# Kernel optimization log

Measured on AMD Instinct MI355X. Metric: run time of the kernel, lower is better.

Reference implementation:

```python
import jax, jax.numpy as jnp
import numpy as np

H = 1024      # hidden_size
I = 512       # moe_intermediate_size
E = 8         # n_routed_experts
K = 2         # num_experts_per_tok
SI = I * 2    # shared expert intermediate (n_shared_experts=2)
B, S = 2, 1024


def setup_inputs() -> dict:
    key = jax.random.key(0)
    ks = jax.random.split(key, 9)
    s = 0.02
    return {
        "x": jax.random.normal(ks[0], (B, S, H), jnp.float32),
        "gate_w": jax.random.normal(ks[1], (E, H), jnp.float32) * s,
        "lb_bias": jnp.zeros((E,), jnp.float32),
        "expert_gate_w": jax.random.normal(ks[2], (E, I, H), jnp.float32) * s,
        "expert_up_w": jax.random.normal(ks[3], (E, I, H), jnp.float32) * s,
        "expert_down_w": jax.random.normal(ks[4], (E, H, I), jnp.float32) * s,
        "shared_gate_w": jax.random.normal(ks[5], (SI, H), jnp.float32) * s,
        "shared_up_w": jax.random.normal(ks[6], (SI, H), jnp.float32) * s,
        "shared_down_w": jax.random.normal(ks[7], (H, SI), jnp.float32) * s,
    }


def _mlp(x, gw, uw, dw):
    # SwiGLU: down( silu(gate(x)) * up(x) )
    return (jax.nn.silu(x @ gw.T) * (x @ uw.T)) @ dw.T


def reference(x, gate_w, lb_bias, expert_gate_w, expert_up_w, expert_down_w,
              shared_gate_w, shared_up_w, shared_down_w):
    b, s, h = x.shape
    xf = x.reshape(-1, h)                                   # [T, H]
    # --- SimpleRouter (sigmoid scoring) ---
    logits = xf @ gate_w.T + lb_bias                        # [T, E]
    scores = jax.nn.sigmoid(logits.astype(jnp.float32))
    topw, topi = jax.lax.top_k(scores, K)                   # [T, K]
    topw = (topw / (topw.sum(-1, keepdims=True) + 1e-8)).astype(x.dtype)
    # --- _process_local: per-expert dispatch/compute/combine ---
    # Faithful to torch source: expert_weights[mask].mean(dim=-1) collapses to a
    # SCALAR per expert (mean routing weight over all tokens sent to that expert).
    out = jnp.zeros_like(xf)
    for e in range(E):
        m = (topi == e)                                     # [T, K]
        sel = m.any(axis=-1)                                # [T]
        cnt = m.sum()
        wmean = (topw * m).sum() / jnp.maximum(cnt, 1).astype(topw.dtype)
        y = _mlp(xf, expert_gate_w[e], expert_up_w[e], expert_down_w[e])  # [T, H]
        out = out + jnp.where(sel[:, None], y * wmean, jnp.zeros((), x.dtype))
    out = out.reshape(b, s, h)
    # --- shared experts ---
    out = out + _mlp(x, shared_gate_w, shared_up_w, shared_down_w)
    return out
```

## Files before the change

### kernel.cpp

```cpp
#include <hip/hip_runtime.h>

#define H_DIM 1024
#define I_DIM 512
#define NE 8
#define SI_DIM 1024
#define NT 2048
#define NS 4096

typedef __bf16 bf16;
typedef __bf16 bf16x4 __attribute__((ext_vector_type(4)));
typedef __bf16 bf16x8 __attribute__((ext_vector_type(8)));
typedef float f32x4 __attribute__((ext_vector_type(4)));

#define OFF_CNT 0
#define OFF_WM 64
#define OFF_TOPI 1024
#define OFF_TOPW (OFF_TOPI + NT * 8)
#define OFF_LISTS (OFF_TOPW + NT * 8)
#define OFF_XB (OFF_LISTS + NE * NT * 4)
#define OFF_ACTE (OFF_XB + (size_t)NT * H_DIM * 2)
#define OFF_ACTS (OFF_ACTE + (size_t)NE * NT * I_DIM * 2)

__device__ __forceinline__ bf16x4 cvt4(f32x4 v) {
  bf16x4 r;
  r.x = (bf16)v.x; r.y = (bf16)v.y; r.z = (bf16)v.z; r.w = (bf16)v.w;
  return r;
}

__device__ __forceinline__ bf16x8 cvt8(f32x4 a, f32x4 b) {
  bf16x8 r;
  r[0] = (bf16)a.x; r[1] = (bf16)a.y; r[2] = (bf16)a.z; r[3] = (bf16)a.w;
  r[4] = (bf16)b.x; r[5] = (bf16)b.y; r[6] = (bf16)b.z; r[7] = (bf16)b.w;
  return r;
}

__device__ __forceinline__ void glds16(const bf16* g, bf16* l) {
  __builtin_amdgcn_global_load_lds(
      (const __attribute__((address_space(1))) unsigned int*)g,
      (__attribute__((address_space(3))) unsigned int*)l, 16, 0, 0);
}

__global__ __launch_bounds__(256) void router_kernel(
    const float* __restrict__ x, const float* __restrict__ gw,
    const float* __restrict__ lb, bf16* __restrict__ xb,
    int2* __restrict__ topi, float2* __restrict__ topw) {
  const int lane = threadIdx.x & 63;
  const int t = blockIdx.x * 4 + (threadIdx.x >> 6);
  const float* xr = x + (size_t)t * H_DIM;
  bf16* xw = xb + (size_t)t * H_DIM;

  float s[NE];
#pragma unroll
  for (int e = 0; e < NE; e++) s[e] = 0.f;
#pragma unroll
  for (int k0 = 0; k0 < H_DIM; k0 += 256) {
    f32x4 xv = *(const f32x4*)(xr + k0 + lane * 4);
    *(bf16x4*)(xw + k0 + lane * 4) = cvt4(xv);
#pragma unroll
    for (int e = 0; e < NE; e++) {
      f32x4 gv = *(const f32x4*)(gw + e * H_DIM + k0 + lane * 4);
      s[e] += xv.x * gv.x + xv.y * gv.y + xv.z * gv.z + xv.w * gv.w;
    }
  }
#pragma unroll
  for (int e = 0; e < NE; e++) {
    float v = s[e];
#pragma unroll
    for (int off = 32; off > 0; off >>= 1) v += __shfl_xor(v, off);
    s[e] = v;
  }
  if (lane == 0) {
    float sc[NE];
#pragma unroll
    for (int e = 0; e < NE; e++) sc[e] = 1.f / (1.f + expf(-(s[e] + lb[e])));
    int i1 = 0;
#pragma unroll
    for (int e = 1; e < NE; e++)
      if (sc[e] > sc[i1]) i1 = e;
    int i2 = -1;
#pragma unroll
    for (int e = 0; e < NE; e++) {
      if (e == i1) continue;
      if (i2 < 0 || sc[e] > sc[i2]) i2 = e;
    }
    float w1 = sc[i1], w2 = sc[i2];
    float inv = 1.f / (w1 + w2 + 1e-8f);
    topi[t] = make_int2(i1, i2);
    topw[t] = make_float2(w1 * inv, w2 * inv);
  }
}

__global__ __launch_bounds__(256) void build_kernel(
    const int2* __restrict__ topi, const float2* __restrict__ topw,
    int* __restrict__ cnt, float* __restrict__ wm, int* __restrict__ lists) {
  const int e = blockIdx.x;
  const int wave = threadIdx.x >> 6, lane = threadIdx.x & 63;
  __shared__ int wc[4];
  __shared__ float wf[4];
  const int tbeg = wave * (NT / 4), tend = tbeg + NT / 4;

  int c = 0;
  float wa = 0.f;
  for (int t0 = tbeg; t0 < tend; t0 += 64) {
    int2 ti = topi[t0 + lane];
    float2 tw = topw[t0 + lane];
    bool hit = (ti.x == e) || (ti.y == e);
    float w = (ti.x == e) ? tw.x : ((ti.y == e) ? tw.y : 0.f);
    c += __popcll(__ballot(hit));
#pragma unroll
    for (int off = 32; off > 0; off >>= 1) w += __shfl_xor(w, off);
    wa += w;
  }
  if (lane == 0) { wc[wave] = c; wf[wave] = wa; }
  __syncthreads();
  int pos = 0;
  for (int w = 0; w < wave; w++) pos += wc[w];
  for (int t0 = tbeg; t0 < tend; t0 += 64) {
    int t = t0 + lane;
    int2 ti = topi[t];
    bool hit = (ti.x == e) || (ti.y == e);
    unsigned long long m = __ballot(hit);
    int pre = __popcll(m & ((1ull << lane) - 1ull));
    if (hit) lists[e * NT + pos + pre] = t;
    pos += __popcll(m);
  }
  if (threadIdx.x == 0) {
    int ctot = wc[0] + wc[1] + wc[2] + wc[3];
    cnt[e] = ctot;
    wm[e] = (wf[0] + wf[1] + wf[2] + wf[3]) / (float)(ctot > 0 ? ctot : 1);
  }
}

__global__ __launch_bounds__(256, 2) void gemm_gu(
    const float* __restrict__ eg, const float* __restrict__ eu,
    const float* __restrict__ sg, const float* __restrict__ su,
    const bf16* __restrict__ xb, const int* __restrict__ cnt,
    const int* __restrict__ lists, bf16* __restrict__ act_e,
    bf16* __restrict__ act_s) {
  const int z = blockIdx.z, ct = blockIdx.x, rt = blockIdx.y;
  const int tid = threadIdx.x;
  __shared__ int rows_s[128];
  __shared__ __align__(16) bf16 As[128 * 64];
  __shared__ __align__(16) bf16 Bs[128 * 64];
  int mrem, ldc;
  bf16* Cb;
  const float *Pg, *Pu;
  if (z < NE) {
    if (ct >= 8) return;
    int c = cnt[z];
    if (rt * 128 >= c) return;
    mrem = c - rt * 128;
    if (tid < 128)
      rows_s[tid] = lists[z * NT + rt * 128 + (tid < mrem ? tid : mrem - 1)];
    Pg = eg + ((size_t)z << 19);
    Pu = eu + ((size_t)z << 19);
    Cb = act_e + ((size_t)z * NT + rt * 128) * I_DIM;
    ldc = I_DIM;
  } else {
    mrem = 128;
    if (tid < 128) rows_s[tid] = rt * 128 + tid;
    Pg = sg;
    Pu = su;
    Cb = act_s + (size_t)rt * 128 * SI_DIM;
    ldc = SI_DIM;
  }
  __syncthreads();

  const int lane = tid & 63, wave = tid >> 6;
  const int mw = (wave >> 1) * 64, nw = (wave & 1) * 64;
  const int l15 = lane & 15, quad = lane >> 4;
  const int srow = tid >> 3;
  const int cch = tid & 7;
  const int p8 = cch * 8;
  const int sx = (l15 & 7) * 8;
  const int ctb = ct * 128;

  const bf16* ap[4];
  const float* bp[4];
  int alo[4], blo[4];
#pragma unroll
  for (int r = 0; r < 4; r++) {
    int R = srow + r * 32;
    ap[r] = xb + (size_t)rows_s[R] * H_DIM + ((cch ^ (R & 7)) * 8);
    alo[r] = R * 64 + p8;
    int idx = ctb + R;
    int b = idx >> 4;
    int sr = ((b >> 1) << 4) | (idx & 15);
    bp[r] = ((b & 1) ? Pu : Pg) + (size_t)sr * H_DIM + p8;
    blo[r] = R * 64 + ((cch ^ (R & 7)) * 8);
  }

  f32x4 acc[4][4] = {};
  for (int k0 = 0; k0 < H_DIM; k0 += 64) {
#pragma unroll
    for (int r = 0; r < 4; r++) glds16(ap[r] + k0, &As[alo[r]]);
#pragma unroll
    for (int r = 0; r < 4; r++) {
      f32x4 v0 = *(const f32x4*)(bp[r] + k0);
      f32x4 v1 = *(const f32x4*)(bp[r] + k0 + 4);
      *(bf16x8*)&Bs[blo[r]] = cvt8(v0, v1);
    }
    __syncthreads();
#pragma unroll
    for (int kk = 0; kk < 2; kk++) {
      const int ko = (kk * 4 + quad) * 8;
      bf16x8 av[4], bv[4];
#pragma unroll
      for (int i = 0; i < 4; i++) {
        av[i] = *(const bf16x8*)&As[(mw + i * 16 + l15) * 64 + (ko ^ sx)];
        bv[i] = *(const bf16x8*)&Bs[(nw + i * 16 + l15) * 64 + (ko ^ sx)];
      }
#pragma unroll
      for (int i = 0; i < 4; i++)
#pragma unroll
        for (int j = 0; j < 4; j++)
          acc[i][j] = __builtin_amdgcn_mfma_f32_16x16x32_bf16(av[i], bv[j], acc[i][j], 0, 0, 0);
    }
    __syncthreads();
  }

#pragma unroll
  for (int i = 0; i < 4; i++) {
#pragma unroll
    for (int rg = 0; rg < 4; rg++) {
      int rl = mw + i * 16 + quad * 4 + rg;
      if (rl < mrem) {
#pragma unroll
        for (int jp = 0; jp < 2; jp++) {
          float g = acc[i][jp * 2][rg];
          float u = acc[i][jp * 2 + 1][rg];
          int c = ct * 64 + (nw >> 1) + jp * 16 + l15;
          Cb[(size_t)rl * ldc + c] = (bf16)((g / (1.f + __expf(-g))) * u);
        }
      }
    }
  }
}

__global__ __launch_bounds__(256, 2) void gemm_down(
    const float* __restrict__ ed, const float* __restrict__ sd,
    const bf16* __restrict__ act_e, const bf16* __restrict__ act_s,
    const int* __restrict__ cnt, const float* __restrict__ wm,
    const int* __restrict__ lists, float* __restrict__ out) {
  const int z = blockIdx.z, ct = blockIdx.x, rt = blockIdx.y;
  const int tid = threadIdx.x;
  __shared__ int rows_s[128];
  __shared__ __align__(16) bf16 As[128 * 64];
  __shared__ __align__(16) bf16 Bs[128 * 64];
  int K, mrem;
  const bf16* Ab;
  const float* Bbase;
  if (z < NE) {
    int c = cnt[z];
    if (rt * 128 >= c) return;
    mrem = c - rt * 128;
    if (tid < 128)
      rows_s[tid] = lists[z * NT + rt * 128 + (tid < mrem ? tid : mrem - 1)];
    Ab = act_e + ((size_t)z * NT + rt * 128) * I_DIM;
    K = I_DIM;
    Bbase = ed + (size_t)z * H_DIM * I_DIM;
  } else {
    mrem = 128;
    if (tid < 128) rows_s[tid] = rt * 128 + tid;
    Ab = act_s + (size_t)rt * 128 * SI_DIM;
    K = SI_DIM;
    Bbase = sd;
  }
  __syncthreads();

  const int lane = tid & 63, wave = tid >> 6;
  const int mw = (wave >> 1) * 64, nw = (wave & 1) * 64;
  const int l15 = lane & 15, quad = lane >> 4;
  const int srow = tid >> 3;
  const int cch = tid & 7;
  const int p8 = cch * 8;
  const int sx = (l15 & 7) * 8;

  const bf16* ap[4];
  const float* bp[4];
  int alo[4], blo[4];
#pragma unroll
  for (int r = 0; r < 4; r++) {
    int R = srow + r * 32;
    ap[r] = Ab + (size_t)R * K + ((cch ^ (R & 7)) * 8);
    alo[r] = R * 64 + p8;
    bp[r] = Bbase + (size_t)(ct * 128 + R) * K + p8;
    blo[r] = R * 64 + ((cch ^ (R & 7)) * 8);
  }

  f32x4 acc[4][4] = {};
  for (int k0 = 0; k0 < K; k0 += 64) {
#pragma unroll
    for (int r = 0; r < 4; r++) glds16(ap[r] + k0, &As[alo[r]]);
#pragma unroll
    for (int r = 0; r < 4; r++) {
      f32x4 v0 = *(const f32x4*)(bp[r] + k0);
      f32x4 v1 = *(const f32x4*)(bp[r] + k0 + 4);
      *(bf16x8*)&Bs[blo[r]] = cvt8(v0, v1);
    }
    __syncthreads();
#pragma unroll
    for (int kk = 0; kk < 2; kk++) {
      const int ko = (kk * 4 + quad) * 8;
      bf16x8 av[4], bv[4];
#pragma unroll
      for (int i = 0; i < 4; i++) {
        av[i] = *(const bf16x8*)&As[(mw + i * 16 + l15) * 64 + (ko ^ sx)];
        bv[i] = *(const bf16x8*)&Bs[(nw + i * 16 + l15) * 64 + (ko ^ sx)];
      }
#pragma unroll
      for (int i = 0; i < 4; i++)
#pragma unroll
        for (int j = 0; j < 4; j++)
          acc[i][j] = __builtin_amdgcn_mfma_f32_16x16x32_bf16(av[i], bv[j], acc[i][j], 0, 0, 0);
    }
    __syncthreads();
  }

  const float wsc = (z < NE) ? wm[z] : 1.f;
#pragma unroll
  for (int i = 0; i < 4; i++) {
#pragma unroll
    for (int rg = 0; rg < 4; rg++) {
      int rl = mw + i * 16 + quad * 4 + rg;
      if (rl < mrem) {
        int t = rows_s[rl];
        float* orow = out + (size_t)t * H_DIM + ct * 128 + nw;
#pragma unroll
        for (int j = 0; j < 4; j++)
          atomicAdd(&orow[j * 16 + l15], wsc * acc[i][j][rg]);
      }
    }
  }
}

extern "C" void kernel_launch(void* const* d_in, const int* in_sizes, int n_in,
                              void* d_out, int out_size, void* d_ws,
                              size_t ws_size, hipStream_t stream) {
  (void)in_sizes; (void)n_in; (void)out_size; (void)ws_size;
  const float* x  = (const float*)d_in[0];
  const float* gw = (const float*)d_in[1];
  const float* lb = (const float*)d_in[2];
  const float* eg = (const float*)d_in[3];
  const float* eu = (const float*)d_in[4];
  const float* ed = (const float*)d_in[5];
  const float* sg = (const float*)d_in[6];
  const float* su = (const float*)d_in[7];
  const float* sd = (const float*)d_in[8];
  float* out = (float*)d_out;
  char* ws = (char*)d_ws;

  int* cnt     = (int*)(ws + OFF_CNT);
  float* wm    = (float*)(ws + OFF_WM);
  int2* topi   = (int2*)(ws + OFF_TOPI);
  float2* topw = (float2*)(ws + OFF_TOPW);
  int* lists   = (int*)(ws + OFF_LISTS);
  bf16* xb     = (bf16*)(ws + OFF_XB);
  bf16* act_e  = (bf16*)(ws + OFF_ACTE);
  bf16* act_s  = (bf16*)(ws + OFF_ACTS);

  hipMemsetAsync(d_out, 0, (size_t)NT * H_DIM * sizeof(float), stream);
  router_kernel<<<NT / 4, 256, 0, stream>>>(x, gw, lb, xb, topi, topw);
  build_kernel<<<NE, 256, 0, stream>>>(topi, topw, cnt, wm, lists);
  gemm_gu<<<dim3(16, 16, 9), 256, 0, stream>>>(eg, eu, sg, su, xb, cnt, lists,
                                               act_e, act_s);
  gemm_down<<<dim3(8, 16, 9), 256, 0, stream>>>(ed, sd, act_e, act_s, cnt, wm,
                                                lists, out);
}
```

Baseline: 209.6 us.

## Pre-convert all expert weights to bf16 once and stream via LDS loads

Adds a weight-conversion pass, merged into the router kernel, that converts all expert and shared weights from fp32 to bf16 in a workspace buffer and pre-interleaves the gate/up rows. The GEMMs then load B tiles with direct global-to-LDS loads instead of fp32 register loads plus conversion, which halves GEMM-side weight bytes. The gate/up GEMM re-reads each weight tile across many row tiles, so much of that re-read traffic is removed. Grid axes are also swapped so row tiles vary fastest for weight reuse in cache. The cost is an extra full pass over about 60MB of fp32 weights every call, writing about 30MB of bf16.

```diff
diff --git a/kernel.cpp b/kernel.cpp
--- a/kernel.cpp
+++ b/kernel.cpp
@@ -5,19 +5,28 @@
 #define NE 8
 #define SI_DIM 1024
 #define NT 2048
-#define NS 4096
 
 typedef __bf16 bf16;
 typedef __bf16 bf16x4 __attribute__((ext_vector_type(4)));
 typedef __bf16 bf16x8 __attribute__((ext_vector_type(8)));
 typedef float f32x4 __attribute__((ext_vector_type(4)));
+
+#define W_GU 0ull
+#define W_DN 8388608ull
+#define W_SGU 12582912ull
+#define W_SDN 14680064ull
+#define W_TOT 15728640ull
+
+#define NWB 15360
+#define NRB 512
 
 #define OFF_CNT 0
 #define OFF_WM 64
 #define OFF_TOPI 1024
 #define OFF_TOPW (OFF_TOPI + NT * 8)
 #define OFF_LISTS (OFF_TOPW + NT * 8)
-#define OFF_XB (OFF_LISTS + NE * NT * 4)
+#define OFF_WB (OFF_LISTS + NE * NT * 4)
+#define OFF_XB (OFF_WB + (size_t)W_TOT * 2)
 #define OFF_ACTE (OFF_XB + (size_t)NT * H_DIM * 2)
 #define OFF_ACTS (OFF_ACTE + (size_t)NE * NT * I_DIM * 2)
 
@@ -27,66 +36,88 @@
   return r;
 }
 
-__device__ __forceinline__ bf16x8 cvt8(f32x4 a, f32x4 b) {
-  bf16x8 r;
-  r[0] = (bf16)a.x; r[1] = (bf16)a.y; r[2] = (bf16)a.z; r[3] = (bf16)a.w;
-  r[4] = (bf16)b.x; r[5] = (bf16)b.y; r[6] = (bf16)b.z; r[7] = (bf16)b.w;
-  return r;
-}
-
 __device__ __forceinline__ void glds16(const bf16* g, bf16* l) {
   __builtin_amdgcn_global_load_lds(
       (const __attribute__((address_space(1))) unsigned int*)g,
       (__attribute__((address_space(3))) unsigned int*)l, 16, 0, 0);
 }
 
-__global__ __launch_bounds__(256) void router_kernel(
+__global__ __launch_bounds__(256) void prep_kernel(
     const float* __restrict__ x, const float* __restrict__ gw,
-    const float* __restrict__ lb, bf16* __restrict__ xb,
-    int2* __restrict__ topi, float2* __restrict__ topw) {
-  const int lane = threadIdx.x & 63;
-  const int t = blockIdx.x * 4 + (threadIdx.x >> 6);
-  const float* xr = x + (size_t)t * H_DIM;
-  bf16* xw = xb + (size_t)t * H_DIM;
-
-  float s[NE];
-#pragma unroll
-  for (int e = 0; e < NE; e++) s[e] = 0.f;
-#pragma unroll
-  for (int k0 = 0; k0 < H_DIM; k0 += 256) {
-    f32x4 xv = *(const f32x4*)(xr + k0 + lane * 4);
-    *(bf16x4*)(xw + k0 + lane * 4) = cvt4(xv);
+    const float* __restrict__ lb, const float* __restrict__ eg,
+    const float* __restrict__ eu, const float* __restrict__ ed,
+    const float* __restrict__ sg, const float* __restrict__ su,
+    const float* __restrict__ sd, bf16* __restrict__ wb,
+    bf16* __restrict__ xb, int2* __restrict__ topi,
+    float2* __restrict__ topw) {
+  const int bx = blockIdx.x;
+  const int tid = threadIdx.x;
+  if (bx < NWB) {
+    size_t i = ((size_t)bx * 256 + tid) * 4;
+    const float* src;
+    if (i < W_DN) {
+      size_t z = i >> 20;
+      int rem = (int)(i & ((1u << 20) - 1));
+      int rp = rem >> 10, k = rem & 1023;
+      int b = rp >> 4;
+      int sr = ((b >> 1) << 4) | (rp & 15);
+      src = ((b & 1) ? eu : eg) + (z << 19) + ((size_t)sr << 10) + k;
+    } else if (i < W_SGU) {
+      src = ed + (i - W_DN);
+    } else if (i < W_SDN) {
+      int rem = (int)(i - W_SGU);
+      int rp = rem >> 10, k = rem & 1023;
+      int b = rp >> 4;
+      int sr = ((b >> 1) << 4) | (rp & 15);
+      src = ((b & 1) ? su : sg) + ((size_t)sr << 10) + k;
+    } else {
+      src = sd + (i - W_SDN);
+    }
+    *(bf16x4*)(wb + i) = cvt4(*(const f32x4*)src);
+  } else {
+    const int lane = tid & 63;
+    const int t = (bx - NWB) * 4 + (tid >> 6);
+    const float* xr = x + (size_t)t * H_DIM;
+    bf16* xw = xb + (size_t)t * H_DIM;
+    float s[NE];
+#pragma unroll
+    for (int e = 0; e < NE; e++) s[e] = 0.f;
+#pragma unroll
+    for (int k0 = 0; k0 < H_DIM; k0 += 256) {
+      f32x4 xv = *(const f32x4*)(xr + k0 + lane * 4);
+      *(bf16x4*)(xw + k0 + lane * 4) = cvt4(xv);
+#pragma unroll
+      for (int e = 0; e < NE; e++) {
+        f32x4 gv = *(const f32x4*)(gw + e * H_DIM + k0 + lane * 4);
+        s[e] += xv.x * gv.x + xv.y * gv.y + xv.z * gv.z + xv.w * gv.w;
+      }
+    }
 #pragma unroll
     for (int e = 0; e < NE; e++) {
-      f32x4 gv = *(const f32x4*)(gw + e * H_DIM + k0 + lane * 4);
-      s[e] += xv.x * gv.x + xv.y * gv.y + xv.z * gv.z + xv.w * gv.w;
-    }
-  }
-#pragma unroll
-  for (int e = 0; e < NE; e++) {
-    float v = s[e];
-#pragma unroll
-    for (int off = 32; off > 0; off >>= 1) v += __shfl_xor(v, off);
-    s[e] = v;
-  }
-  if (lane == 0) {
-    float sc[NE];
-#pragma unroll
-    for (int e = 0; e < NE; e++) sc[e] = 1.f / (1.f + expf(-(s[e] + lb[e])));
-    int i1 = 0;
-#pragma unroll
-    for (int e = 1; e < NE; e++)
-      if (sc[e] > sc[i1]) i1 = e;
-    int i2 = -1;
-#pragma unroll
-    for (int e = 0; e < NE; e++) {
-      if (e == i1) continue;
-      if (i2 < 0 || sc[e] > sc[i2]) i2 = e;
-    }
-    float w1 = sc[i1], w2 = sc[i2];
-    float inv = 1.f / (w1 + w2 + 1e-8f);
-    topi[t] = make_int2(i1, i2);
-    topw[t] = make_float2(w1 * inv, w2 * inv);
+      float v = s[e];
+#pragma unroll
+      for (int off = 32; off > 0; off >>= 1) v += __shfl_xor(v, off);
+      s[e] = v;
+    }
+    if (lane == 0) {
+      float sc[NE];
+#pragma unroll
+      for (int e = 0; e < NE; e++) sc[e] = 1.f / (1.f + expf(-(s[e] + lb[e])));
+      int i1 = 0;
+#pragma unroll
+      for (int e = 1; e < NE; e++)
+        if (sc[e] > sc[i1]) i1 = e;
+      int i2 = -1;
+#pragma unroll
+      for (int e = 0; e < NE; e++) {
+        if (e == i1) continue;
+        if (i2 < 0 || sc[e] > sc[i2]) i2 = e;
+      }
+      float w1 = sc[i1], w2 = sc[i2];
+      float inv = 1.f / (w1 + w2 + 1e-8f);
+      topi[t] = make_int2(i1, i2);
+      topw[t] = make_float2(w1 * inv, w2 * inv);
+    }
   }
 }
 
@@ -132,19 +163,17 @@
 }
 
 __global__ __launch_bounds__(256, 2) void gemm_gu(
-    const float* __restrict__ eg, const float* __restrict__ eu,
-    const float* __restrict__ sg, const float* __restrict__ su,
-    const bf16* __restrict__ xb, const int* __restrict__ cnt,
-    const int* __restrict__ lists, bf16* __restrict__ act_e,
-    bf16* __restrict__ act_s) {
-  const int z = blockIdx.z, ct = blockIdx.x, rt = blockIdx.y;
+    const bf16* __restrict__ wb, const bf16* __restrict__ xb,
+    const int* __restrict__ cnt, const int* __restrict__ lists,
+    bf16* __restrict__ act_e, bf16* __restrict__ act_s) {
+  const int z = blockIdx.z, rt = blockIdx.x, ct = blockIdx.y;
   const int tid = threadIdx.x;
   __shared__ int rows_s[128];
   __shared__ __align__(16) bf16 As[128 * 64];
   __shared__ __align__(16) bf16 Bs[128 * 64];
   int mrem, ldc;
   bf16* Cb;
-  const float *Pg, *Pu;
+  const bf16* Bb;
   if (z < NE) {
     if (ct >= 8) return;
     int c = cnt[z];
@@ -152,15 +181,13 @@
     mrem = c - rt * 128;
     if (tid < 128)
       rows_s[tid] = lists[z * NT + rt * 128 + (tid < mrem ? tid : mrem - 1)];
-    Pg = eg + ((size_t)z << 19);
-    Pu = eu + ((size_t)z << 19);
+    Bb = wb + W_GU + ((size_t)z << 20) + (size_t)ct * 128 * H_DIM;
     Cb = act_e + ((size_t)z * NT + rt * 128) * I_DIM;
     ldc = I_DIM;
   } else {
     mrem = 128;
     if (tid < 128) rows_s[tid] = rt * 128 + tid;
-    Pg = sg;
-    Pu = su;
+    Bb = wb + W_SGU + (size_t)ct * 128 * H_DIM;
     Cb = act_s + (size_t)rt * 128 * SI_DIM;
     ldc = SI_DIM;
   }
@@ -173,33 +200,24 @@
   const int cch = tid & 7;
   const int p8 = cch * 8;
   const int sx = (l15 & 7) * 8;
-  const int ctb = ct * 128;
-
-  const bf16* ap[4];
-  const float* bp[4];
-  int alo[4], blo[4];
+
+  const bf16 *ap[4], *bp[4];
+  int lo[4];
 #pragma unroll
   for (int r = 0; r < 4; r++) {
     int R = srow + r * 32;
-    ap[r] = xb + (size_t)rows_s[R] * H_DIM + ((cch ^ (R & 7)) * 8);
-    alo[r] = R * 64 + p8;
-    int idx = ctb + R;
-    int b = idx >> 4;
-    int sr = ((b >> 1) << 4) | (idx & 15);
-    bp[r] = ((b & 1) ? Pu : Pg) + (size_t)sr * H_DIM + p8;
-    blo[r] = R * 64 + ((cch ^ (R & 7)) * 8);
+    int gs = (cch ^ (R & 7)) * 8;
+    ap[r] = xb + (size_t)rows_s[R] * H_DIM + gs;
+    bp[r] = Bb + (size_t)R * H_DIM + gs;
+    lo[r] = R * 64 + p8;
   }
 
   f32x4 acc[4][4] = {};
   for (int k0 = 0; k0 < H_DIM; k0 += 64) {
 #pragma unroll
-    for (int r = 0; r < 4; r++) glds16(ap[r] + k0, &As[alo[r]]);
-#pragma unroll
-    for (int r = 0; r < 4; r++) {
-      f32x4 v0 = *(const f32x4*)(bp[r] + k0);
-      f32x4 v1 = *(const f32x4*)(bp[r] + k0 + 4);
-      *(bf16x8*)&Bs[blo[r]] = cvt8(v0, v1);
-    }
+    for (int r = 0; r < 4; r++) glds16(ap[r] + k0, &As[lo[r]]);
+#pragma unroll
+    for (int r = 0; r < 4; r++) glds16(bp[r] + k0, &Bs[lo[r]]);
     __syncthreads();
 #pragma unroll
     for (int kk = 0; kk < 2; kk++) {
@@ -238,18 +256,17 @@
 }
 
 __global__ __launch_bounds__(256, 2) void gemm_down(
-    const float* __restrict__ ed, const float* __restrict__ sd,
-    const bf16* __restrict__ act_e, const bf16* __restrict__ act_s,
-    const int* __restrict__ cnt, const float* __restrict__ wm,
-    const int* __restrict__ lists, float* __restrict__ out) {
-  const int z = blockIdx.z, ct = blockIdx.x, rt = blockIdx.y;
+    const bf16* __restrict__ wb, const bf16* __restrict__ act_e,
+    const bf16* __restrict__ act_s, const int* __restrict__ cnt,
+    const float* __restrict__ wm, const int* __restrict__ lists,
+    float* __restrict__ out) {
+  const int z = blockIdx.z, rt = blockIdx.x, ct = blockIdx.y;
   const int tid = threadIdx.x;
   __shared__ int rows_s[128];
   __shared__ __align__(16) bf16 As[128 * 64];
   __shared__ __align__(16) bf16 Bs[128 * 64];
   int K, mrem;
-  const bf16* Ab;
-  const float* Bbase;
+  const bf16 *Ab, *Bb;
   if (z < NE) {
     int c = cnt[z];
     if (rt * 128 >= c) return;
@@ -258,13 +275,13 @@
       rows_s[tid] = lists[z * NT + rt * 128 + (tid < mrem ? tid : mrem - 1)];
     Ab = act_e + ((size_t)z * NT + rt * 128) * I_DIM;
     K = I_DIM;
-    Bbase = ed + (size_t)z * H_DIM * I_DIM;
+    Bb = wb + W_DN + ((size_t)z << 19) + (size_t)ct * 128 * I_DIM;
   } else {
     mrem = 128;
     if (tid < 128) rows_s[tid] = rt * 128 + tid;
     Ab = act_s + (size_t)rt * 128 * SI_DIM;
     K = SI_DIM;
-    Bbase = sd;
+    Bb = wb + W_SDN + (size_t)ct * 128 * SI_DIM;
   }
   __syncthreads();
 
@@ -276,28 +293,23 @@
   const int p8 = cch * 8;
   const int sx = (l15 & 7) * 8;
 
-  const bf16* ap[4];
-  const float* bp[4];
-  int alo[4], blo[4];
+  const bf16 *ap[4], *bp[4];
+  int lo[4];
 #pragma unroll
   for (int r = 0; r < 4; r++) {
     int R = srow + r * 32;
-    ap[r] = Ab + (size_t)R * K + ((cch ^ (R & 7)) * 8);
-    alo[r] = R * 64 + p8;
-    bp[r] = Bbase + (size_t)(ct * 128 + R) * K + p8;
-    blo[r] = R * 64 + ((cch ^ (R & 7)) * 8);
+    int gs = (cch ^ (R & 7)) * 8;
+    ap[r] = Ab + (size_t)R * K + gs;
+    bp[r] = Bb + (size_t)R * K + gs;
+    lo[r] = R * 64 + p8;
   }
 
   f32x4 acc[4][4] = {};
   for (int k0 = 0; k0 < K; k0 += 64) {
 #pragma unroll
-    for (int r = 0; r < 4; r++) glds16(ap[r] + k0, &As[alo[r]]);
-#pragma unroll
-    for (int r = 0; r < 4; r++) {
-      f32x4 v0 = *(const f32x4*)(bp[r] + k0);
-      f32x4 v1 = *(const f32x4*)(bp[r] + k0 + 4);
-      *(bf16x8*)&Bs[blo[r]] = cvt8(v0, v1);
-    }
+    for (int r = 0; r < 4; r++) glds16(ap[r] + k0, &As[lo[r]]);
+#pragma unroll
+    for (int r = 0; r < 4; r++) glds16(bp[r] + k0, &Bs[lo[r]]);
     __syncthreads();
 #pragma unroll
     for (int kk = 0; kk < 2; kk++) {
@@ -355,15 +367,17 @@
   int2* topi   = (int2*)(ws + OFF_TOPI);
   float2* topw = (float2*)(ws + OFF_TOPW);
   int* lists   = (int*)(ws + OFF_LISTS);
+  bf16* wb     = (bf16*)(ws + OFF_WB);
   bf16* xb     = (bf16*)(ws + OFF_XB);
   bf16* act_e  = (bf16*)(ws + OFF_ACTE);
   bf16* act_s  = (bf16*)(ws + OFF_ACTS);
 
   hipMemsetAsync(d_out, 0, (size_t)NT * H_DIM * sizeof(float), stream);
-  router_kernel<<<NT / 4, 256, 0, stream>>>(x, gw, lb, xb, topi, topw);
+  prep_kernel<<<NWB + NRB, 256, 0, stream>>>(x, gw, lb, eg, eu, ed, sg, su, sd,
+                                             wb, xb, topi, topw);
   build_kernel<<<NE, 256, 0, stream>>>(topi, topw, cnt, wm, lists);
-  gemm_gu<<<dim3(16, 16, 9), 256, 0, stream>>>(eg, eu, sg, su, xb, cnt, lists,
-                                               act_e, act_s);
-  gemm_down<<<dim3(8, 16, 9), 256, 0, stream>>>(ed, sd, act_e, act_s, cnt, wm,
+  gemm_gu<<<dim3(16, 16, 9), 256, 0, stream>>>(wb, xb, cnt, lists, act_e,
+                                               act_s);
+  gemm_down<<<dim3(16, 8, 9), 256, 0, stream>>>(wb, act_e, act_s, cnt, wm,
                                                 lists, out);
 }
```

Result: slower. 216.0 us (+3.1%).
